# Performance work log

Hardware: AMD Instinct MI355X
Metric: run time of the kernel (lower is better)

The kernel has to match this reference:

```python
import jax, jax.numpy as jnp
import numpy as np

# dims: B batch, L residues, CS=c_s, N_EXP mHC streams, H heads, CH c_hidden,
# PQK/PV qk/v points, CZ=c_p pair channels, RANK z-factor rank, CZQ=CZ//4
B, L, CS, N_EXP, H, CH, PQK, PV, CZ, RANK = 4, 1024, 384, 4, 8, 64, 4, 8, 128, 2
CZQ = CZ // 4
SINKHORN_ITERS = 20


def quat_to_rot(q):
    q = q / jnp.sqrt((q * q).sum(-1, keepdims=True) + 1e-8)
    w, x, y, z = q[..., 0], q[..., 1], q[..., 2], q[..., 3]
    R = jnp.stack([
        1 - 2 * (y * y + z * z), 2 * (x * y - w * z), 2 * (x * z + w * y),
        2 * (x * y + w * z), 1 - 2 * (x * x + z * z), 2 * (y * z - w * x),
        2 * (x * z - w * y), 2 * (y * z + w * x), 1 - 2 * (x * x + y * y)], axis=-1)
    return R.reshape(q.shape[:-1] + (3, 3))


def layer_norm(x, g, b, eps=1e-5):
    mu = x.mean(-1, keepdims=True)
    var = ((x - mu) ** 2).mean(-1, keepdims=True)
    return (x - mu) * jax.lax.rsqrt(var + eps) * g + b


def sinkhorn(logits):
    # project onto doubly-stochastic matrices (Birkhoff polytope), fixed iters
    M = jnp.exp(logits - logits.max(axis=(-2, -1), keepdims=True))
    for _ in range(SINKHORN_ITERS):
        M = M / (M.sum(-1, keepdims=True) + 1e-8)
        M = M / (M.sum(-2, keepdims=True) + 1e-8)
    return M


def _forward(s, z_factor_1, z_factor_2, quat_t, trans, mask, b_pre, b_post, b_res,
             W_pre, W_post, W_res, alpha, Wq, Wk, Wv, Wq_pts, Wk_pts, Wv_pts,
             Wz_q, Wz_k, head_w, Wo, bo, ln1_g, ln1_b, Wt1, bt1, Wt2, bt2,
             Wt3, bt3, lnt_g, lnt_b, Wbb, bbb):
    # --- mHC: expand_input (first layer replicates stream) + dynamic mappings ---
    s_exp = jnp.broadcast_to(s[:, :, None, :], (B, L, N_EXP, CS))
    h = s_exp.reshape(B, L, N_EXP * CS)
    hn = h * jax.lax.rsqrt((h * h).mean(-1, keepdims=True) + 1e-6)
    H_pre = jax.nn.softmax(b_pre + alpha * (hn @ W_pre), -1)        # [B,L,n]
    H_post = 2.0 * jax.nn.sigmoid(b_post + alpha * (hn @ W_post))   # [B,L,n]
    H_res = sinkhorn(b_res + alpha * (hn @ W_res).reshape(B, L, N_EXP, N_EXP))
    s_c = jnp.einsum('bln,blnc->blc', H_pre, s_exp)                 # contraction

    rot = quat_to_rot(quat_t)                                       # [B,L,3,3]

    # --- Flash-IPA (dense math-equivalent reference) ---
    q = (s_c @ Wq).reshape(B, L, H, CH)
    k = (s_c @ Wk).reshape(B, L, H, CH)
    v = (s_c @ Wv).reshape(B, L, H, CH)
    qp = (s_c @ Wq_pts).reshape(B, L, H, PQK, 3)
    kp = (s_c @ Wk_pts).reshape(B, L, H, PQK, 3)
    vp = (s_c @ Wv_pts).reshape(B, L, H, PV, 3)

    def to_global(p):
        return jnp.einsum('blij,blhpj->blhpi', rot, p) + trans[:, :, None, None, :]

    qp_g, kp_g, vp_g = to_global(qp), to_global(kp), to_global(vp)

    # low-rank factorized pair bias (z = outer product of per-residue factors)
    zq = jnp.einsum('blrz,zh->blrh', z_factor_1, Wz_q)
    zk = jnp.einsum('blrz,zh->blrh', z_factor_1, Wz_k)
    bias = jnp.einsum('birh,bjrh->bhij', zq, zk)

    qk = jnp.einsum('bihc,bjhc->bhij', q, k) / np.sqrt(CH)
    qn = (qp_g ** 2).sum((-2, -1)).transpose(0, 2, 1)               # [B,H,L]
    kn = (kp_g ** 2).sum((-2, -1)).transpose(0, 2, 1)
    pdot = jnp.einsum('bihpd,bjhpd->bhij', qp_g, kp_g)
    d2 = qn[:, :, :, None] + kn[:, :, None, :] - 2.0 * pdot         # sum_p ||qp_i - kp_j||^2
    gamma = jax.nn.softplus(head_w)
    wC = np.sqrt(2.0 / (9.0 * PQK))
    wL = np.sqrt(1.0 / 3.0)
    logits = wL * (qk + bias) - (wL * wC * 0.5) * gamma[None, :, None, None] * d2
    logits = jnp.where(mask[:, None, None, :] > 0, logits, -1e9)
    a = jax.nn.softmax(logits, -1)

    o = jnp.einsum('bhij,bjhc->bihc', a, v).reshape(B, L, H * CH)
    opt_g = jnp.einsum('bhij,bjhpd->bihpd', a, vp_g)
    diff = opt_g - trans[:, :, None, None, :]
    opt_l = jnp.einsum('blij,blhpi->blhpj', rot, diff)              # R^T (x - t)
    opt_norm = jnp.sqrt((opt_l ** 2).sum(-1) + 1e-8)
    opair = jnp.einsum('bhij,bjhrc->bihrc', a, z_factor_2).reshape(B, L, H * RANK * CZQ)
    feat = jnp.concatenate([o, opt_l.reshape(B, L, H * PV * 3),
                            opt_norm.reshape(B, L, H * PV), opair], -1)
    ipa_out = feat @ Wo + bo

    # residual + (dropout=identity at eval) + LN + transition (residual MLP) + LN
    s1 = layer_norm(s_c + ipa_out, ln1_g, ln1_b)
    t1 = jax.nn.relu(s1 @ Wt1 + bt1)
    t2 = jax.nn.relu(t1 @ Wt2 + bt2)
    s_ipa = layer_norm(s1 + (t2 @ Wt3 + bt3), lnt_g, lnt_b)

    # backbone update: quaternion (1,b,c,d) + translation, composed with frame
    upd = s_ipa @ Wbb + bbb                                         # [B,L,6]
    quat_u = jnp.concatenate([jnp.ones((B, L, 1), upd.dtype), upd[..., :3]], -1)
    R_u = quat_to_rot(quat_u)
    rot_new = jnp.einsum('blij,bljk->blik', rot, R_u)
    trans_new = jnp.einsum('blij,blj->bli', rot, upd[..., 3:]) + trans

    # mHC combine: H_res @ s  +  H_post^T * s_ipa (broadcast over streams)
    s_out = jnp.einsum('blmn,blnc->blmc', H_res, s_exp) + H_post[..., None] * s_ipa[:, :, None, :]
    return s_out, rot_new, trans_new


def setup_inputs() -> dict:
    key = jax.random.key(0)
    ks = jax.random.split(key, 24)

    def nrm(k, shape, scale=1.0):
        return jax.random.normal(k, shape, jnp.float32) * scale

    FEAT = H * CH + H * PV * 4 + H * RANK * CZQ  # 512 + 256 + 512 = 1280
    return dict(
        s=nrm(ks[0], (B, L, CS)),
        z_factor_1=nrm(ks[1], (B, L, RANK, CZ)),
        z_factor_2=nrm(ks[2], (B, L, H, RANK, CZQ)),
        quat_t=nrm(ks[3], (B, L, 4)),
        trans=nrm(ks[4], (B, L, 3)),
        mask=jnp.ones((B, L), jnp.float32),
        b_pre=nrm(ks[5], (N_EXP,), 0.02),
        b_post=nrm(ks[6], (N_EXP,), 0.02),
        b_res=nrm(ks[7], (N_EXP, N_EXP), 0.02),
        W_pre=nrm(ks[8], (N_EXP * CS, N_EXP), 0.02),
        W_post=nrm(ks[9], (N_EXP * CS, N_EXP), 0.02),
        W_res=nrm(ks[10], (N_EXP * CS, N_EXP * N_EXP), 0.02),
        alpha=jnp.float32(0.01),
        Wq=nrm(ks[11], (CS, H * CH), 0.02),
        Wk=nrm(ks[12], (CS, H * CH), 0.02),
        Wv=nrm(ks[13], (CS, H * CH), 0.02),
        Wq_pts=nrm(ks[14], (CS, H * PQK * 3), 0.02),
        Wk_pts=nrm(ks[15], (CS, H * PQK * 3), 0.02),
        Wv_pts=nrm(ks[16], (CS, H * PV * 3), 0.02),
        Wz_q=nrm(ks[17], (CZ, H), 0.02),
        Wz_k=nrm(ks[18], (CZ, H), 0.02),
        head_w=jnp.zeros((H,), jnp.float32),
        Wo=nrm(ks[19], (FEAT, CS), 0.02),
        bo=jnp.zeros((CS,), jnp.float32),
        ln1_g=jnp.ones((CS,), jnp.float32),
        ln1_b=jnp.zeros((CS,), jnp.float32),
        Wt1=nrm(ks[20], (CS, CS), 0.02),
        bt1=jnp.zeros((CS,), jnp.float32),
        Wt2=nrm(ks[21], (CS, CS), 0.02),
        bt2=jnp.zeros((CS,), jnp.float32),
        Wt3=nrm(ks[22], (CS, CS), 0.02),
        bt3=jnp.zeros((CS,), jnp.float32),
        lnt_g=jnp.ones((CS,), jnp.float32),
        lnt_b=jnp.zeros((CS,), jnp.float32),
        Wbb=nrm(ks[23], (CS, 6), 0.02),
        bbb=jnp.zeros((6,), jnp.float32),
    )


def reference(s, z_factor_1, z_factor_2, quat_t, trans, mask, b_pre, b_post, b_res,
              W_pre, W_post, W_res, alpha, Wq, Wk, Wv, Wq_pts, Wk_pts, Wv_pts,
              Wz_q, Wz_k, head_w, Wo, bo, ln1_g, ln1_b, Wt1, bt1, Wt2, bt2,
              Wt3, bt3, lnt_g, lnt_b, Wbb, bbb):
    return _forward(s, z_factor_1, z_factor_2, quat_t, trans, mask, b_pre, b_post,
                    b_res, W_pre, W_post, W_res, alpha, Wq, Wk, Wv, Wq_pts, Wk_pts,
                    Wv_pts, Wz_q, Wz_k, head_w, Wo, bo, ln1_g, ln1_b, Wt1, bt1,
                    Wt2, bt2, Wt3, bt3, lnt_g, lnt_b, Wbb, bbb)
```

## Files before the change

### kernel.cpp

```cpp
#include <hip/hip_runtime.h>
#include <hip/hip_bf16.h>

typedef __hip_bfloat16 bf16;
typedef float f4v __attribute__((ext_vector_type(4)));
typedef short s8v __attribute__((ext_vector_type(8)));

#define CSD    384
#define LL     1024
#define NH     8
#define BL     4096
#define NPROJ  1920
#define QDP    96
#define VDP    160
#define FEATD  1280

#define OFF_S      0
#define OFF_QUAT   1572864
#define OFF_TRANS  1589248
#define OFF_MASK   1601536
#define OFF_BPOST  1605632
#define OFF_BRES   1605648
#define OFF_WPOST  1605664
#define OFF_WRES   1611808
#define OFF_ALPHA  1636384
#define OFF_WQ     1636400
#define OFF_WK     1833008
#define OFF_WV     2029616
#define OFF_WQP    2226224
#define OFF_WKP    2263088
#define OFF_WVP    2299952
#define OFF_WZQ    2373680
#define OFF_WZK    2374704
#define OFF_HEADW  2375728
#define OFF_WO     2375744
#define OFF_BO     2867264
#define OFF_LN1G   2867648
#define OFF_LN1B   2868032
#define OFF_WT1    2868416
#define OFF_BT1    3015872
#define OFF_WT2    3016256
#define OFF_BT2    3163712
#define OFF_WT3    3164096
#define OFF_BT3    3311552
#define OFF_LNTG   3311936
#define OFF_LNTB   3312320
#define OFF_WBB    3312704
#define OFF_BBB    3315008
#define IN_END     3315024

#define WS_FLAG    3315024
#define WS_WPOSTR  3315040
#define WS_WRESR   3316576
#define WS_HPOST   3322720
#define WS_ROWSUM  3339104
#define WS_ROTB    3355488
#define WS_WCATT   3392352
#define WS_WOT     3760992
#define WS_WT1T    4006752
#define WS_WT2T    4080480
#define WS_WT3T    4154208
#define WS_PROJ    4227936
#define WS_QB      12092256
#define WS_KB      13665120
#define WS_VT      15237984

#define OUT_ROT 6291456
#define OUT_TR  6328320

#define NSEG 32

struct P36 { const void* p[36]; };

__device__ __forceinline__ float b2f(bf16 x) { return __bfloat162float(x); }

__device__ __forceinline__ short f2bs(float x) {
  unsigned u = __float_as_uint(x);
  u += 0x7FFFu + ((u >> 16) & 1u);
  return (short)(u >> 16);
}

__device__ __forceinline__ int packbf(float lo, float hi) {
  return (int)(unsigned short)f2bs(lo) | ((int)f2bs(hi) << 16);
}

__device__ __forceinline__ float ldraw(const void* p, size_t i, int flag) {
  return flag ? b2f(((const bf16*)p)[i]) : ((const float*)p)[i];
}

__device__ __forceinline__ float wredf(float v) {
#pragma unroll
  for (int o = 1; o < 64; o <<= 1) v += __shfl_xor(v, o, 64);
  return v;
}

__global__ void detect_k(const unsigned int* __restrict__ mask_raw, int* __restrict__ flag) {
  if (threadIdx.x == 0 && blockIdx.x == 0) flag[0] = (mask_raw[0] == 0x3F803F80u) ? 1 : 0;
}

__global__ __launch_bounds__(256) void cvtall_k(P36 ptrs, float* __restrict__ dst, const int* __restrict__ flagp) {
  const int i = blockIdx.x * 256 + threadIdx.x;
  if (i >= IN_END) return;
  const int flag = flagp[0];
  const int seg_src_t[NSEG] = {0,3,4,5,7,8,10,11,12,13,14,15,16,17,18,19,20,21,22,23,24,25,26,27,28,29,30,31,32,33,34,35};
  const int seg_dst_t[NSEG] = {OFF_S,OFF_QUAT,OFF_TRANS,OFF_MASK,OFF_BPOST,OFF_BRES,OFF_WPOST,OFF_WRES,OFF_ALPHA,
                               OFF_WQ,OFF_WK,OFF_WV,OFF_WQP,OFF_WKP,OFF_WVP,OFF_WZQ,OFF_WZK,OFF_HEADW,
                               OFF_WO,OFF_BO,OFF_LN1G,OFF_LN1B,OFF_WT1,OFF_BT1,OFF_WT2,OFF_BT2,OFF_WT3,OFF_BT3,
                               OFF_LNTG,OFF_LNTB,OFF_WBB,OFF_BBB};
  const int seg_cnt_t[NSEG] = {1572864,16384,12288,4096,4,16,6144,24576,1,
                               196608,196608,196608,36864,36864,73728,1024,1024,8,
                               491520,384,384,384,147456,384,147456,384,147456,384,
                               384,384,2304,6};
  int off = i, cnt = seg_cnt_t[0];
  const void* sp = ptrs.p[0];
#pragma unroll
  for (int k = 1; k < NSEG; k++) {
    if (i >= seg_dst_t[k]) { off = i - seg_dst_t[k]; cnt = seg_cnt_t[k]; sp = ptrs.p[seg_src_t[k]]; }
  }
  float v = 0.f;
  if (off < cnt) v = flag ? b2f(((const bf16*)sp)[off]) : ((const float*)sp)[off];
  dst[i] = v;
}

__global__ __launch_bounds__(256) void wprep_k(const float* __restrict__ ws, short* __restrict__ wsS) {
  const int jobs_src[10] = {OFF_WQ, OFF_WK, OFF_WV, OFF_WQP, OFF_WKP, OFF_WVP, OFF_WO, OFF_WT1, OFF_WT2, OFF_WT3};
  const int jobs_dst[10] = {WS_WCATT*2, WS_WCATT*2 + 512*384, WS_WCATT*2 + 1024*384, WS_WCATT*2 + 1536*384,
                            WS_WCATT*2 + 1632*384, WS_WCATT*2 + 1728*384, WS_WOT*2, WS_WT1T*2, WS_WT2T*2, WS_WT3T*2};
  const int jobs_K[10] = {384,384,384,384,384,384,1280,384,384,384};
  const int jobs_N[10] = {512,512,512,96,96,192,384,384,384,384};
  const int jobs_t0[10] = {0,192,384,576,612,648,720,1200,1344,1488};
  const int t = blockIdx.x;
  int j = 0;
#pragma unroll
  for (int k = 1; k < 10; k++) if (t >= jobs_t0[k]) j = k;
  const int tl = t - jobs_t0[j];
  const int K = jobs_K[j], N = jobs_N[j];
  const int ntn = N >> 5;
  const int kt = tl / ntn, nt = tl - kt * ntn;
  const int k0 = kt * 32, n0 = nt * 32;
  const float* src = ws + jobs_src[j];
  short* dst = wsS + jobs_dst[j];
  __shared__ float T[32][36];
  {
    const int r = threadIdx.x >> 3, cq = (threadIdx.x & 7) * 4;
    const float4 a = *(const float4*)(src + (size_t)(k0 + r) * N + n0 + cq);
    T[r][cq] = a.x; T[r][cq + 1] = a.y; T[r][cq + 2] = a.z; T[r][cq + 3] = a.w;
  }
  __syncthreads();
  {
    const int n = threadIdx.x >> 3, kq = (threadIdx.x & 7) * 4;
    short pk4[4];
#pragma unroll
    for (int e = 0; e < 4; e++) pk4[e] = f2bs(T[kq + e][n]);
    *(int2*)(dst + (size_t)(n0 + n) * K + k0 + kq) = *(const int2*)pk4;
  }
}

__global__ __launch_bounds__(256) void wreduce_k(const float* __restrict__ Wpost, const float* __restrict__ Wres,
                                                 float* __restrict__ WpostR, float* __restrict__ WresR) {
  int i = blockIdx.x * 256 + threadIdx.x;
  if (i < CSD * 4) {
    int c = i >> 2, n = i & 3;
    float s = 0.f;
#pragma unroll
    for (int blk = 0; blk < 4; blk++) s += Wpost[(blk * CSD + c) * 4 + n];
    WpostR[i] = s;
  }
  if (i < CSD * 16) {
    int c = i >> 4, n = i & 15;
    float s = 0.f;
#pragma unroll
    for (int blk = 0; blk < 4; blk++) s += Wres[(blk * CSD + c) * 16 + n];
    WresR[i] = s;
  }
}

__global__ __launch_bounds__(64) void mhc_k(const float* __restrict__ sF, const float* __restrict__ quat,
                                            const float* __restrict__ bpost, const float* __restrict__ bres,
                                            const float* __restrict__ alpha_p, const float* __restrict__ WpostR,
                                            const float* __restrict__ WresR, float* __restrict__ hpost,
                                            float* __restrict__ rowsum, float* __restrict__ rotb) {
  const int bl = blockIdx.x, t = threadIdx.x;
  const float* sr = sF + (size_t)bl * CSD;
  float ssq = 0.f, dp[4] = {0.f, 0.f, 0.f, 0.f}, dr[16];
#pragma unroll
  for (int n = 0; n < 16; n++) dr[n] = 0.f;
#pragma unroll
  for (int e = 0; e < 6; e++) {
    const int c = t + e * 64;
    const float sv = sr[c];
    ssq = fmaf(sv, sv, ssq);
#pragma unroll
    for (int n = 0; n < 4; n++) dp[n] = fmaf(sv, WpostR[c * 4 + n], dp[n]);
#pragma unroll
    for (int n = 0; n < 16; n++) dr[n] = fmaf(sv, WresR[c * 16 + n], dr[n]);
  }
  ssq = wredf(ssq);
#pragma unroll
  for (int n = 0; n < 4; n++) dp[n] = wredf(dp[n]);
#pragma unroll
  for (int n = 0; n < 16; n++) dr[n] = wredf(dr[n]);
  const float alpha = alpha_p[0];
  const float invn = rsqrtf(ssq * (1.f / 384.f) + 1e-6f);
  if (t == 0) {
#pragma unroll
    for (int n = 0; n < 4; n++) {
      const float x = bpost[n] + alpha * invn * dp[n];
      hpost[bl * 4 + n] = 2.f / (1.f + __expf(-x));
    }
    float M[16];
    float mx = -1e30f;
#pragma unroll
    for (int k = 0; k < 16; k++) { M[k] = bres[k] + alpha * invn * dr[k]; mx = fmaxf(mx, M[k]); }
#pragma unroll
    for (int k = 0; k < 16; k++) M[k] = __expf(M[k] - mx);
    for (int it = 0; it < 20; it++) {
#pragma unroll
      for (int r = 0; r < 4; r++) {
        const float s4 = M[r * 4] + M[r * 4 + 1] + M[r * 4 + 2] + M[r * 4 + 3];
        const float iv = 1.f / (s4 + 1e-8f);
        M[r * 4] *= iv; M[r * 4 + 1] *= iv; M[r * 4 + 2] *= iv; M[r * 4 + 3] *= iv;
      }
#pragma unroll
      for (int c2 = 0; c2 < 4; c2++) {
        const float s4 = M[c2] + M[4 + c2] + M[8 + c2] + M[12 + c2];
        const float iv = 1.f / (s4 + 1e-8f);
        M[c2] *= iv; M[4 + c2] *= iv; M[8 + c2] *= iv; M[12 + c2] *= iv;
      }
    }
#pragma unroll
    for (int r = 0; r < 4; r++)
      rowsum[bl * 4 + r] = M[r * 4] + M[r * 4 + 1] + M[r * 4 + 2] + M[r * 4 + 3];
  }
  if (t == 1) {
    float w = quat[bl * 4 + 0], x = quat[bl * 4 + 1];
    float y = quat[bl * 4 + 2], z = quat[bl * 4 + 3];
    const float iq = rsqrtf(w * w + x * x + y * y + z * z + 1e-8f);
    w *= iq; x *= iq; y *= iq; z *= iq;
    float* R = rotb + (size_t)bl * 9;
    R[0] = 1.f - 2.f * (y * y + z * z); R[1] = 2.f * (x * y - w * z); R[2] = 2.f * (x * z + w * y);
    R[3] = 2.f * (x * y + w * z); R[4] = 1.f - 2.f * (x * x + z * z); R[5] = 2.f * (y * z - w * x);
    R[6] = 2.f * (x * z - w * y); R[7] = 2.f * (y * z + w * x); R[8] = 1.f - 2.f * (x * x + y * y);
  }
}

__global__ __launch_bounds__(256) void gemm_mfma_k(const float* __restrict__ A, const short* __restrict__ Bt,
                                                   const float* __restrict__ bias, float* __restrict__ C,
                                                   int M, int N, int K, int relu) {
  __shared__ __align__(16) short As[128 * 40];
  __shared__ __align__(16) short Bs[128 * 40];
  const int tid = threadIdx.x;
  const int wid = tid >> 6, lane = tid & 63;
  const int c15 = lane & 15, q = lane >> 4;
  const int bm = blockIdx.y, bn = blockIdx.x;
  const int m_wave = (wid & 1) * 64, n_wave = (wid >> 1) * 64;
  const float* Ab = A + (size_t)(bm * 128) * K;
  const short* Bb = Bt + (size_t)(bn * 128) * K;

  f4v acc[4][4];
#pragma unroll
  for (int mi = 0; mi < 4; mi++)
#pragma unroll
    for (int ni = 0; ni < 4; ni++) acc[mi][ni] = (f4v){0.f, 0.f, 0.f, 0.f};

  for (int k0 = 0; k0 < K; k0 += 32) {
    __syncthreads();
#pragma unroll
    for (int e = 0; e < 4; e++) {
      const int slot = tid + e * 256;
      const int m = slot >> 3, k4 = (slot & 7) * 4;
      const float4 a = *(const float4*)(Ab + (size_t)m * K + k0 + k4);
      short pk[4] = {f2bs(a.x), f2bs(a.y), f2bs(a.z), f2bs(a.w)};
      *(int2*)&As[m * 40 + k4] = *(const int2*)pk;
    }
#pragma unroll
    for (int e = 0; e < 2; e++) {
      const int slot = tid + e * 256;
      const int n = slot >> 2, k8 = (slot & 3) * 8;
      *(int4*)&Bs[n * 40 + k8] = *(const int4*)(Bb + (size_t)n * K + k0 + k8);
    }
    __syncthreads();
    s8v Af[4], Bf[4];
#pragma unroll
    for (int mi = 0; mi < 4; mi++) Af[mi] = *(const s8v*)&As[(m_wave + mi * 16 + c15) * 40 + q * 8];
#pragma unroll
    for (int ni = 0; ni < 4; ni++) Bf[ni] = *(const s8v*)&Bs[(n_wave + ni * 16 + c15) * 40 + q * 8];
#pragma unroll
    for (int mi = 0; mi < 4; mi++)
#pragma unroll
      for (int ni = 0; ni < 4; ni++)
        acc[mi][ni] = __builtin_amdgcn_mfma_f32_16x16x32_bf16(Af[mi], Bf[ni], acc[mi][ni], 0, 0, 0);
  }
#pragma unroll
  for (int mi = 0; mi < 4; mi++) {
#pragma unroll
    for (int r = 0; r < 4; r++) {
      const int row = bm * 128 + m_wave + mi * 16 + q * 4 + r;
      float* Cr = C + (size_t)row * N + bn * 128 + n_wave;
#pragma unroll
      for (int ni = 0; ni < 4; ni++) {
        const int col = bn * 128 + n_wave + ni * 16 + c15;
        float v = acc[mi][ni][r];
        if (bias != nullptr) v += bias[col];
        if (relu) v = fmaxf(v, 0.f);
        Cr[ni * 16 + c15] = v;
      }
    }
  }
}

__global__ __launch_bounds__(64) void assemble_k(const float* __restrict__ proj, const float* __restrict__ rotb,
                                                 const float* __restrict__ trans, const void* __restrict__ z1raw,
                                                 const void* __restrict__ z2raw, const float* __restrict__ Wzq,
                                                 const float* __restrict__ Wzk, const float* __restrict__ headw,
                                                 const int* __restrict__ flagp, short* __restrict__ Qb,
                                                 short* __restrict__ Kb, short* __restrict__ Vtb) {
  __shared__ float qt[8][16], kt[8][16];
  const int bl = blockIdx.x, lane = threadIdx.x;
  const int h = lane >> 3, sub = lane & 7;
  const int flag = flagp[0];
  const float* pr = proj + (size_t)bl * NPROJ;
  const float* R = rotb + (size_t)bl * 9;
  const float txx = trans[bl * 3 + 0], tyy = trans[bl * 3 + 1], tzz = trans[bl * 3 + 2];
  float gamma;
  { const float w = headw[h]; gamma = (w > 20.f) ? w : log1pf(__expf(w)); }
  const float wL = 0.57735026918962576f;
  const float wC = 0.23570226039551584f;
  const float ch = wL * wC * 0.5f * gamma;
  const float qscale = wL * 0.125f;

  float zq0 = 0.f, zq1 = 0.f, zk0 = 0.f, zk1 = 0.f;
  const size_t zbase = (size_t)bl * 256;
  for (int zz = sub; zz < 128; zz += 8) {
    const float a0 = ldraw(z1raw, zbase + zz, flag);
    const float a1 = ldraw(z1raw, zbase + 128 + zz, flag);
    const float wq = Wzq[zz * 8 + h], wk = Wzk[zz * 8 + h];
    zq0 = fmaf(a0, wq, zq0); zq1 = fmaf(a1, wq, zq1);
    zk0 = fmaf(a0, wk, zk0); zk1 = fmaf(a1, wk, zk1);
  }
#pragma unroll
  for (int o = 1; o < 8; o <<= 1) {
    zq0 += __shfl_xor(zq0, o, 64); zq1 += __shfl_xor(zq1, o, 64);
    zk0 += __shfl_xor(zk0, o, 64); zk1 += __shfl_xor(zk1, o, 64);
  }

  const int b = bl >> 10, l = bl & 1023;
  const int bh = b * NH + h;
  const size_t row = (size_t)bh * LL + l;
  short* Q = Qb + row * QDP;
  short* Kx = Kb + row * QDP;

  {
    const float* ps = pr + h * 64 + sub * 8;
    const float4 a0 = ((const float4*)ps)[0], a1 = ((const float4*)ps)[1];
    int4 qi;
    qi.x = packbf(a0.x * qscale, a0.y * qscale); qi.y = packbf(a0.z * qscale, a0.w * qscale);
    qi.z = packbf(a1.x * qscale, a1.y * qscale); qi.w = packbf(a1.z * qscale, a1.w * qscale);
    ((int4*)Q)[sub] = qi;
    const float* pk = pr + 512 + h * 64 + sub * 8;
    const float4 b0 = ((const float4*)pk)[0], b1 = ((const float4*)pk)[1];
    int4 ki;
    ki.x = packbf(b0.x, b0.y); ki.y = packbf(b0.z, b0.w);
    ki.z = packbf(b1.x, b1.y); ki.w = packbf(b1.z, b1.w);
    ((int4*)Kx)[sub] = ki;
    const float* pv = pr + 1024 + h * 64 + sub * 8;
#pragma unroll
    for (int e = 0; e < 8; e++)
      Vtb[((size_t)bh * VDP + sub * 8 + e) * LL + l] = f2bs(pv[e]);
  }

  {
    const float* pp = pr + ((sub < 4) ? 1536 : 1632) + h * 12 + (sub & 3) * 3;
    const float gx = R[0] * pp[0] + R[1] * pp[1] + R[2] * pp[2] + txx;
    const float gy = R[3] * pp[0] + R[4] * pp[1] + R[5] * pp[2] + tyy;
    const float gz = R[6] * pp[0] + R[7] * pp[1] + R[8] * pp[2] + tzz;
    float nrm = gx * gx + gy * gy + gz * gz;
    nrm += __shfl_xor(nrm, 1, 64);
    nrm += __shfl_xor(nrm, 2, 64);
    const float other = __shfl_xor(nrm, 4, 64);
    const float qn = (sub < 4) ? nrm : other;
    const float kn = (sub < 4) ? other : nrm;
    if (sub < 4) {
      qt[h][2 + sub * 3 + 0] = 2.f * ch * gx;
      qt[h][2 + sub * 3 + 1] = 2.f * ch * gy;
      qt[h][2 + sub * 3 + 2] = 2.f * ch * gz;
    } else {
      kt[h][2 + (sub - 4) * 3 + 0] = gx;
      kt[h][2 + (sub - 4) * 3 + 1] = gy;
      kt[h][2 + (sub - 4) * 3 + 2] = gz;
    }
    if (sub == 0) {
      qt[h][0] = wL * zq0; qt[h][1] = wL * zq1; qt[h][14] = -ch * qn; qt[h][15] = 1.f;
      kt[h][0] = zk0;      kt[h][1] = zk1;      kt[h][14] = 1.f;      kt[h][15] = -ch * kn;
    }
  }
  {
    int4 z4; z4.x = 0; z4.y = 0; z4.z = 0; z4.w = 0;
    if (sub < 2) {
      const float* s4 = &qt[h][sub * 8];
      int4 qi;
      qi.x = packbf(s4[0], s4[1]); qi.y = packbf(s4[2], s4[3]);
      qi.z = packbf(s4[4], s4[5]); qi.w = packbf(s4[6], s4[7]);
      ((int4*)Q)[8 + sub] = qi;
    } else if (sub < 4) {
      const float* s4 = &kt[h][(sub - 2) * 8];
      int4 ki;
      ki.x = packbf(s4[0], s4[1]); ki.y = packbf(s4[2], s4[3]);
      ki.z = packbf(s4[4], s4[5]); ki.w = packbf(s4[6], s4[7]);
      ((int4*)Kx)[8 + sub - 2] = ki;
    } else if (sub == 4) ((int4*)Q)[10] = z4;
    else if (sub == 5) ((int4*)Q)[11] = z4;
    else if (sub == 6) ((int4*)Kx)[10] = z4;
    else ((int4*)Kx)[11] = z4;
  }
  {
    const float* pv3 = pr + 1728 + h * 24 + sub * 3;
    const float gx = R[0] * pv3[0] + R[1] * pv3[1] + R[2] * pv3[2] + txx;
    const float gy = R[3] * pv3[0] + R[4] * pv3[1] + R[5] * pv3[2] + tyy;
    const float gz = R[6] * pv3[0] + R[7] * pv3[1] + R[8] * pv3[2] + tzz;
    const int c = 64 + sub * 3;
    Vtb[((size_t)bh * VDP + c + 0) * LL + l] = f2bs(gx);
    Vtb[((size_t)bh * VDP + c + 1) * LL + l] = f2bs(gy);
    Vtb[((size_t)bh * VDP + c + 2) * LL + l] = f2bs(gz);
  }
  {
    const size_t z2base = ((size_t)bl * NH + h) * 64 + sub * 8;
#pragma unroll
    for (int e = 0; e < 8; e++)
      Vtb[((size_t)bh * VDP + 88 + sub * 8 + e) * LL + l] = f2bs(ldraw(z2raw, z2base + e, flag));
    Vtb[((size_t)bh * VDP + 152 + sub) * LL + l] = 0;
  }
}

__global__ __launch_bounds__(512, 2) void attn_k(const short* __restrict__ Qb, const short* __restrict__ Kb,
                                                 const short* __restrict__ Vtb, const float* __restrict__ maskF,
                                                 float* __restrict__ Oext) {
  __shared__ __align__(16) short smem[26624];
  short* Ks = smem;
  short* Vs = smem + 6656;
  short* Ps = smem + 19456;
  float* Msl = (float*)(smem + 24576);
  const int tid = threadIdx.x;
  const int wid = tid >> 6, lane = tid & 63;
  const int c15 = lane & 15, q = lane >> 4;
  const int blk = blockIdx.x;
  const int bh = blk & 31, qt2 = blk >> 5;
  const int b = bh >> 3, h = bh & 7;
  const int half = wid >> 2, mw = wid & 3;
  const int i0 = qt2 * 64 + mw * 16;

  const short* Kbase = Kb + (size_t)bh * LL * QDP;
  const short* Vbase = Vtb + (size_t)bh * VDP * LL;

  s8v Qa[3];
  const short* Qrow = Qb + ((size_t)bh * LL + i0 + c15) * QDP;
#pragma unroll
  for (int kc = 0; kc < 3; kc++) Qa[kc] = *(const s8v*)(Qrow + kc * 32 + q * 8);

  f4v Of[10];
#pragma unroll
  for (int vt = 0; vt < 10; vt++) Of[vt] = (f4v){0.f, 0.f, 0.f, 0.f};
  float mold[4] = {-1e30f, -1e30f, -1e30f, -1e30f};
  float lsum[4] = {0.f, 0.f, 0.f, 0.f};

  Msl[tid] = maskF[b * LL + tid];
  Msl[tid + 512] = maskF[b * LL + tid + 512];

  const int khs0 = tid / 384;
  const int kv0 = tid - khs0 * 384;
  const int krr0 = kv0 / 12, kcc0 = kv0 - krr0 * 12;
  int khs1 = 0, krr1 = 0, kcc1 = 0;
  if (tid < 256) { const int u = tid + 512; khs1 = u / 384; const int v2 = u - khs1 * 384; krr1 = v2 / 12; kcc1 = v2 - krr1 * 12; }
  const int vhs0 = tid / 640; const int vv0 = tid - vhs0 * 640; const int vcc0 = vv0 >> 2, vp0 = vv0 & 3;
  const int vhs1 = (tid + 512) / 640; const int vv1 = (tid + 512) - vhs1 * 640; const int vcc1 = vv1 >> 2, vp1 = vv1 & 3;
  int vhs2 = 0, vcc2 = 0, vp2 = 0;
  if (tid < 256) { const int u = tid + 1024; vhs2 = u / 640; const int v2 = u - vhs2 * 640; vcc2 = v2 >> 2; vp2 = v2 & 3; }

  int4 kr0, kr1, vr0, vr1, vr2;
  kr0 = *(const int4*)(Kbase + (size_t)(khs0 * 512 + krr0) * QDP + kcc0 * 8);
  if (tid < 256) kr1 = *(const int4*)(Kbase + (size_t)(khs1 * 512 + krr1) * QDP + kcc1 * 8);
  vr0 = *(const int4*)(Vbase + (size_t)vcc0 * LL + vhs0 * 512 + vp0 * 8);
  vr1 = *(const int4*)(Vbase + (size_t)vcc1 * LL + vhs1 * 512 + vp1 * 8);
  if (tid < 256) vr2 = *(const int4*)(Vbase + (size_t)vcc2 * LL + vhs2 * 512 + vp2 * 8);

  short* Ksl = Ks + half * 3328;
  short* Vsl = Vs + half * 6400;
  short* Pl = Ps + wid * 640;

  for (int jt = 0; jt < 16; jt++) {
    const int j0 = jt * 32;
    __syncthreads();
    *(int4*)&Ks[khs0 * 3328 + krr0 * 104 + kcc0 * 8] = kr0;
    if (tid < 256) *(int4*)&Ks[khs1 * 3328 + krr1 * 104 + kcc1 * 8] = kr1;
    *(int4*)&Vs[vhs0 * 6400 + vcc0 * 40 + vp0 * 8] = vr0;
    *(int4*)&Vs[vhs1 * 6400 + vcc1 * 40 + vp1 * 8] = vr1;
    if (tid < 256) *(int4*)&Vs[vhs2 * 6400 + vcc2 * 40 + vp2 * 8] = vr2;
    __syncthreads();
    if (jt < 15) {
      const int j0n = j0 + 32;
      kr0 = *(const int4*)(Kbase + (size_t)(khs0 * 512 + j0n + krr0) * QDP + kcc0 * 8);
      if (tid < 256) kr1 = *(const int4*)(Kbase + (size_t)(khs1 * 512 + j0n + krr1) * QDP + kcc1 * 8);
      vr0 = *(const int4*)(Vbase + (size_t)vcc0 * LL + vhs0 * 512 + j0n + vp0 * 8);
      vr1 = *(const int4*)(Vbase + (size_t)vcc1 * LL + vhs1 * 512 + j0n + vp1 * 8);
      if (tid < 256) vr2 = *(const int4*)(Vbase + (size_t)vcc2 * LL + vhs2 * 512 + j0n + vp2 * 8);
    }

    f4v Sf0 = (f4v){0.f, 0.f, 0.f, 0.f}, Sf1 = (f4v){0.f, 0.f, 0.f, 0.f};
#pragma unroll
    for (int kc = 0; kc < 3; kc++) {
      const s8v K0 = *(const s8v*)&Ksl[c15 * 104 + kc * 32 + q * 8];
      const s8v K1 = *(const s8v*)&Ksl[(16 + c15) * 104 + kc * 32 + q * 8];
      Sf0 = __builtin_amdgcn_mfma_f32_16x16x32_bf16(Qa[kc], K0, Sf0, 0, 0, 0);
      Sf1 = __builtin_amdgcn_mfma_f32_16x16x32_bf16(Qa[kc], K1, Sf1, 0, 0, 0);
    }
    const float mv0 = Msl[half * 512 + j0 + c15];
    const float mv1 = Msl[half * 512 + j0 + 16 + c15];
    float lg0[4], lg1[4], tm[4], p0[4], p1[4];
#pragma unroll
    for (int r = 0; r < 4; r++) {
      lg0[r] = (mv0 > 0.f) ? Sf0[r] : -1e9f;
      lg1[r] = (mv1 > 0.f) ? Sf1[r] : -1e9f;
      tm[r] = fmaxf(lg0[r], lg1[r]);
    }
#pragma unroll
    for (int r = 0; r < 4; r++) {
      tm[r] = fmaxf(tm[r], __shfl_xor(tm[r], 1, 64));
      tm[r] = fmaxf(tm[r], __shfl_xor(tm[r], 2, 64));
      tm[r] = fmaxf(tm[r], __shfl_xor(tm[r], 4, 64));
      tm[r] = fmaxf(tm[r], __shfl_xor(tm[r], 8, 64));
    }
    const bool need = (tm[0] > mold[0]) | (tm[1] > mold[1]) | (tm[2] > mold[2]) | (tm[3] > mold[3]);
    if (__any(need)) {
      float al[4];
#pragma unroll
      for (int r = 0; r < 4; r++) {
        const float mn = fmaxf(mold[r], tm[r]);
        al[r] = __expf(mold[r] - mn);
        mold[r] = mn;
        p0[r] = __expf(lg0[r] - mn);
        p1[r] = __expf(lg1[r] - mn);
        lsum[r] = lsum[r] * al[r] + p0[r] + p1[r];
      }
#pragma unroll
      for (int vt = 0; vt < 10; vt++) {
#pragma unroll
        for (int r = 0; r < 4; r++) Of[vt][r] *= al[r];
      }
    } else {
#pragma unroll
      for (int r = 0; r < 4; r++) {
        p0[r] = __expf(lg0[r] - mold[r]);
        p1[r] = __expf(lg1[r] - mold[r]);
        lsum[r] += p0[r] + p1[r];
      }
    }
#pragma unroll
    for (int r = 0; r < 4; r++) {
      Pl[(q * 4 + r) * 40 + c15] = f2bs(p0[r]);
      Pl[(q * 4 + r) * 40 + 16 + c15] = f2bs(p1[r]);
    }
    const s8v Pa = *(const s8v*)&Pl[c15 * 40 + q * 8];
#pragma unroll
    for (int vt = 0; vt < 10; vt++) {
      const s8v Vf = *(const s8v*)&Vsl[(vt * 16 + c15) * 40 + q * 8];
      Of[vt] = __builtin_amdgcn_mfma_f32_16x16x32_bf16(Pa, Vf, Of[vt], 0, 0, 0);
    }
  }
#pragma unroll
  for (int r = 0; r < 4; r++) {
    lsum[r] += __shfl_xor(lsum[r], 1, 64);
    lsum[r] += __shfl_xor(lsum[r], 2, 64);
    lsum[r] += __shfl_xor(lsum[r], 4, 64);
    lsum[r] += __shfl_xor(lsum[r], 8, 64);
  }
  float* Obuf = (float*)smem;
  float* Mbuf = (float*)(smem + 20480);
  float* Lbuf = Mbuf + 64;
  __syncthreads();
  if (half == 1) {
#pragma unroll
    for (int r = 0; r < 4; r++) {
      const int rowi = mw * 16 + q * 4 + r;
#pragma unroll
      for (int vt = 0; vt < 10; vt++) Obuf[rowi * 160 + vt * 16 + c15] = Of[vt][r];
      if (c15 == 0) { Mbuf[rowi] = mold[r]; Lbuf[rowi] = lsum[r]; }
    }
  }
  __syncthreads();
  if (half == 0) {
#pragma unroll
    for (int r = 0; r < 4; r++) {
      const int rowi = mw * 16 + q * 4 + r;
      const float m2 = Mbuf[rowi], l2 = Lbuf[rowi];
      const float mx = fmaxf(mold[r], m2);
      const float a1 = __expf(mold[r] - mx), a2 = __expf(m2 - mx);
      const float inv = 1.f / (lsum[r] * a1 + l2 * a2);
      const int i = i0 + q * 4 + r;
      float* Or = Oext + ((size_t)(b * LL + i) * NH + h) * VDP;
#pragma unroll
      for (int vt = 0; vt < 10; vt++)
        Or[vt * 16 + c15] = (Of[vt][r] * a1 + Obuf[rowi * 160 + vt * 16 + c15] * a2) * inv;
    }
  }
}

__global__ __launch_bounds__(64) void feat_k(const float* __restrict__ Oext, const float* __restrict__ rotb,
                                             const float* __restrict__ trans, float* __restrict__ feat) {
  const int bl = blockIdx.x, lane = threadIdx.x;
  const int h = lane >> 3, sub = lane & 7;
  const float* O = Oext + ((size_t)bl * 8 + h) * VDP;
  float* f = feat + (size_t)bl * FEATD;
  {
    const float4 a0 = ((const float4*)(O + sub * 8))[0], a1 = ((const float4*)(O + sub * 8))[1];
    ((float4*)(f + h * 64 + sub * 8))[0] = a0;
    ((float4*)(f + h * 64 + sub * 8))[1] = a1;
    const float4 z0 = ((const float4*)(O + 88 + sub * 8))[0], z1 = ((const float4*)(O + 88 + sub * 8))[1];
    ((float4*)(f + 768 + h * 64 + sub * 8))[0] = z0;
    ((float4*)(f + 768 + h * 64 + sub * 8))[1] = z1;
  }
  const float* R = rotb + (size_t)bl * 9;
  const float txx = trans[bl * 3 + 0], tyy = trans[bl * 3 + 1], tzz = trans[bl * 3 + 2];
  {
    const float dx = O[64 + sub * 3 + 0] - txx;
    const float dy = O[64 + sub * 3 + 1] - tyy;
    const float dz = O[64 + sub * 3 + 2] - tzz;
    const float lx = R[0] * dx + R[3] * dy + R[6] * dz;
    const float ly = R[1] * dx + R[4] * dy + R[7] * dz;
    const float lz = R[2] * dx + R[5] * dy + R[8] * dz;
    f[512 + h * 24 + sub * 3 + 0] = lx;
    f[512 + h * 24 + sub * 3 + 1] = ly;
    f[512 + h * 24 + sub * 3 + 2] = lz;
    f[704 + h * 8 + sub] = sqrtf(lx * lx + ly * ly + lz * lz + 1e-8f);
  }
}

__global__ __launch_bounds__(64) void ln_k(const float* __restrict__ x, const float* __restrict__ resid,
                                           const float* __restrict__ g, const float* __restrict__ bta,
                                           float* __restrict__ out) {
  const int row = blockIdx.x, t = threadIdx.x;
  const float* xr = x + (size_t)row * CSD;
  const float* rr = resid + (size_t)row * CSD;
  float v[6];
  float s = 0.f;
#pragma unroll
  for (int e = 0; e < 6; e++) {
    const int c = t + e * 64;
    v[e] = xr[c] + rr[c];
    s += v[e];
  }
  s = wredf(s);
  const float mu = s * (1.f / 384.f);
  float var = 0.f;
#pragma unroll
  for (int e = 0; e < 6; e++) { const float d = v[e] - mu; var = fmaf(d, d, var); }
  var = wredf(var) * (1.f / 384.f);
  const float inv = rsqrtf(var + 1e-5f);
#pragma unroll
  for (int e = 0; e < 6; e++) {
    const int c = t + e * 64;
    out[(size_t)row * CSD + c] = (v[e] - mu) * inv * g[c] + bta[c];
  }
}

__global__ __launch_bounds__(64) void lnfinal_k(const float* __restrict__ x , const float* __restrict__ resid ,
                                                const float* __restrict__ g, const float* __restrict__ bta,
                                                const float* __restrict__ sF, const float* __restrict__ rotb,
                                                const float* __restrict__ trans, const float* __restrict__ hpost,
                                                const float* __restrict__ rowsum, const float* __restrict__ Wbb,
                                                const float* __restrict__ bbb, const int* __restrict__ flagp,
                                                void* __restrict__ outv) {
  const int bl = blockIdx.x, t = threadIdx.x;
  const int flag = flagp[0];
  bf16* outb = (bf16*)outv;
  float* outf = (float*)outv;
  const float* xr = x + (size_t)bl * CSD;
  const float* rr = resid + (size_t)bl * CSD;
  float v[6];
  float s = 0.f;
#pragma unroll
  for (int e = 0; e < 6; e++) {
    const int c = t + e * 64;
    v[e] = xr[c] + rr[c];
    s += v[e];
  }
  s = wredf(s);
  const float mu = s * (1.f / 384.f);
  float var = 0.f;
#pragma unroll
  for (int e = 0; e < 6; e++) { const float d = v[e] - mu; var = fmaf(d, d, var); }
  var = wredf(var) * (1.f / 384.f);
  const float inv = rsqrtf(var + 1e-5f);
  float si6[6];
#pragma unroll
  for (int e = 0; e < 6; e++) {
    const int c = t + e * 64;
    si6[e] = (v[e] - mu) * inv * g[c] + bta[c];
  }
  float d6[6] = {0.f, 0.f, 0.f, 0.f, 0.f, 0.f};
#pragma unroll
  for (int e = 0; e < 6; e++) {
    const int c = t + e * 64;
#pragma unroll
    for (int u = 0; u < 6; u++) d6[u] = fmaf(si6[e], Wbb[c * 6 + u], d6[u]);
  }
#pragma unroll
  for (int u = 0; u < 6; u++) d6[u] = wredf(d6[u]);
  float upd[6];
#pragma unroll
  for (int u = 0; u < 6; u++) upd[u] = d6[u] + bbb[u];
  const float* R = rotb + (size_t)bl * 9;
  if (t == 0) {
    float w = 1.f, x2 = upd[0], y = upd[1], z = upd[2];
    const float iq = rsqrtf(w * w + x2 * x2 + y * y + z * z + 1e-8f);
    w *= iq; x2 *= iq; y *= iq; z *= iq;
    const float Ru[9] = {1.f - 2.f * (y * y + z * z), 2.f * (x2 * y - w * z), 2.f * (x2 * z + w * y),
                         2.f * (x2 * y + w * z), 1.f - 2.f * (x2 * x2 + z * z), 2.f * (y * z - w * x2),
                         2.f * (x2 * z - w * y), 2.f * (y * z + w * x2), 1.f - 2.f * (x2 * x2 + y * y)};
#pragma unroll
    for (int i = 0; i < 3; i++)
#pragma unroll
      for (int j = 0; j < 3; j++) {
        const float rv = R[i * 3 + 0] * Ru[0 + j] + R[i * 3 + 1] * Ru[3 + j] + R[i * 3 + 2] * Ru[6 + j];
        const size_t o = OUT_ROT + (size_t)bl * 9 + i * 3 + j;
        if (flag) outb[o] = __float2bfloat16(rv); else outf[o] = rv;
      }
#pragma unroll
    for (int i = 0; i < 3; i++) {
      const float tv = R[i * 3 + 0] * upd[3] + R[i * 3 + 1] * upd[4] + R[i * 3 + 2] * upd[5] + trans[bl * 3 + i];
      const size_t o = OUT_TR + (size_t)bl * 3 + i;
      if (flag) outb[o] = __float2bfloat16(tv); else outf[o] = tv;
    }
  }
  const float hp0 = hpost[bl * 4 + 0], hp1 = hpost[bl * 4 + 1], hp2 = hpost[bl * 4 + 2], hp3 = hpost[bl * 4 + 3];
  const float rs0 = rowsum[bl * 4 + 0], rs1 = rowsum[bl * 4 + 1], rs2 = rowsum[bl * 4 + 2], rs3 = rowsum[bl * 4 + 3];
  const float* sr = sF + (size_t)bl * CSD;
#pragma unroll
  for (int e = 0; e < 6; e++) {
    const int c = t + e * 64;
    const float sv = sr[c], sp = si6[e];
    const size_t base = (size_t)bl * 4 * CSD + c;
    const float o0 = rs0 * sv + hp0 * sp;
    const float o1 = rs1 * sv + hp1 * sp;
    const float o2 = rs2 * sv + hp2 * sp;
    const float o3 = rs3 * sv + hp3 * sp;
    if (flag) {
      outb[base + 0 * CSD] = __float2bfloat16(o0);
      outb[base + 1 * CSD] = __float2bfloat16(o1);
      outb[base + 2 * CSD] = __float2bfloat16(o2);
      outb[base + 3 * CSD] = __float2bfloat16(o3);
    } else {
      outf[base + 0 * CSD] = o0;
      outf[base + 1 * CSD] = o1;
      outf[base + 2 * CSD] = o2;
      outf[base + 3 * CSD] = o3;
    }
  }
}

extern "C" void kernel_launch(void* const* d_in, const int* in_sizes, int n_in,
                              void* d_out, int out_size, void* d_ws, size_t ws_size,
                              hipStream_t stream) {
  float* ws = (float*)d_ws;
  int* flag = (int*)(ws + WS_FLAG);

  P36 ptrs;
  for (int i = 0; i < 36; i++) ptrs.p[i] = d_in[i];

  float* sF     = ws + OFF_S;
  float* WpostR = ws + WS_WPOSTR;
  float* WresR  = ws + WS_WRESR;
  float* hpost  = ws + WS_HPOST;
  float* rowsum = ws + WS_ROWSUM;
  float* rotb   = ws + WS_ROTB;
  short* WcatT  = (short*)(ws + WS_WCATT);
  short* WoT    = (short*)(ws + WS_WOT);
  short* Wt1T   = (short*)(ws + WS_WT1T);
  short* Wt2T   = (short*)(ws + WS_WT2T);
  short* Wt3T   = (short*)(ws + WS_WT3T);
  float* proj   = ws + WS_PROJ;
  short* Qb     = (short*)(ws + WS_QB);
  short* Kb     = (short*)(ws + WS_KB);
  short* Vtb    = (short*)(ws + WS_VT);
  float* Oext   = ws + WS_PROJ;
  float* featb  = ws + WS_QB;
  float* x1s1   = ws + WS_PROJ;
  float* t1b    = ws + WS_PROJ + 1572864;
  float* t2b    = ws + WS_PROJ + 3145728;
  float* x3     = ws + WS_PROJ + 4718592;

  detect_k<<<1, 64, 0, stream>>>((const unsigned int*)d_in[5], flag);
  cvtall_k<<<(IN_END + 255) / 256, 256, 0, stream>>>(ptrs, ws, flag);
  wprep_k<<<1632, 256, 0, stream>>>(ws, (short*)ws);
  wreduce_k<<<24, 256, 0, stream>>>(ws + OFF_WPOST, ws + OFF_WRES, WpostR, WresR);
  mhc_k<<<BL, 64, 0, stream>>>(sF, ws + OFF_QUAT, ws + OFF_BPOST, ws + OFF_BRES, ws + OFF_ALPHA,
                               WpostR, WresR, hpost, rowsum, rotb);
  gemm_mfma_k<<<dim3(15, 32), 256, 0, stream>>>(sF, WcatT, nullptr, proj, BL, NPROJ, CSD, 0);
  assemble_k<<<BL, 64, 0, stream>>>(proj, rotb, ws + OFF_TRANS, d_in[1], d_in[2],
                                    ws + OFF_WZQ, ws + OFF_WZK, ws + OFF_HEADW, flag, Qb, Kb, Vtb);
  attn_k<<<512, 512, 0, stream>>>(Qb, Kb, Vtb, ws + OFF_MASK, Oext);
  feat_k<<<BL, 64, 0, stream>>>(Oext, rotb, ws + OFF_TRANS, featb);
  gemm_mfma_k<<<dim3(3, 32), 256, 0, stream>>>(featb, WoT, ws + OFF_BO, x1s1, BL, CSD, FEATD, 0);
  ln_k<<<BL, 64, 0, stream>>>(x1s1, sF, ws + OFF_LN1G, ws + OFF_LN1B, x1s1);
  gemm_mfma_k<<<dim3(3, 32), 256, 0, stream>>>(x1s1, Wt1T, ws + OFF_BT1, t1b, BL, CSD, CSD, 1);
  gemm_mfma_k<<<dim3(3, 32), 256, 0, stream>>>(t1b, Wt2T, ws + OFF_BT2, t2b, BL, CSD, CSD, 1);
  gemm_mfma_k<<<dim3(3, 32), 256, 0, stream>>>(t2b, Wt3T, ws + OFF_BT3, x3, BL, CSD, CSD, 0);
  lnfinal_k<<<BL, 64, 0, stream>>>(x3, x1s1, ws + OFF_LNTG, ws + OFF_LNTB, sF, rotb,
                                   ws + OFF_TRANS, hpost, rowsum, ws + OFF_WBB, ws + OFF_BBB,
                                   flag, d_out);
}
```

Baseline: 482.3 us.

## Write V row-major in assemble_k and transpose via LDS in new kernel

assemble_k used to write V directly in transposed layout with scattered 2-byte stores at stride LL. It now packs V rows into 16-byte vector stores in a row-major staging buffer. A new vtrans_k kernel then transposes each 64-row tile through shared memory into the layout attn_k expects. This trades uncoalesced scattered stores for one extra kernel launch and an extra read and write of V.

```diff
diff --git a/kernel.cpp b/kernel.cpp
--- a/kernel.cpp
+++ b/kernel.cpp
@@ -63,6 +63,7 @@
 #define WS_QB      12092256
 #define WS_KB      13665120
 #define WS_VT      15237984
+#define WS_VROW    17859424
 
 #define OUT_ROT 6291456
 #define OUT_TR  6328320
@@ -313,8 +314,8 @@
                                                  const void* __restrict__ z2raw, const float* __restrict__ Wzq,
                                                  const float* __restrict__ Wzk, const float* __restrict__ headw,
                                                  const int* __restrict__ flagp, short* __restrict__ Qb,
-                                                 short* __restrict__ Kb, short* __restrict__ Vtb) {
-  __shared__ float qt[8][16], kt[8][16];
+                                                 short* __restrict__ Kb, short* __restrict__ Vrow) {
+  __shared__ float qt[8][16], kt[8][16], vt[8][24];
   const int bl = blockIdx.x, lane = threadIdx.x;
   const int h = lane >> 3, sub = lane & 7;
   const int flag = flagp[0];
@@ -348,6 +349,7 @@
   const size_t row = (size_t)bh * LL + l;
   short* Q = Qb + row * QDP;
   short* Kx = Kb + row * QDP;
+  short* Vo = Vrow + row * VDP;
 
   {
     const float* ps = pr + h * 64 + sub * 8;
@@ -363,9 +365,11 @@
     ki.z = packbf(b1.x, b1.y); ki.w = packbf(b1.z, b1.w);
     ((int4*)Kx)[sub] = ki;
     const float* pv = pr + 1024 + h * 64 + sub * 8;
-#pragma unroll
-    for (int e = 0; e < 8; e++)
-      Vtb[((size_t)bh * VDP + sub * 8 + e) * LL + l] = f2bs(pv[e]);
+    const float4 v0 = ((const float4*)pv)[0], v1 = ((const float4*)pv)[1];
+    int4 vi;
+    vi.x = packbf(v0.x, v0.y); vi.y = packbf(v0.z, v0.w);
+    vi.z = packbf(v1.x, v1.y); vi.w = packbf(v1.z, v1.w);
+    ((int4*)Vo)[sub] = vi;
   }
 
   {
@@ -394,6 +398,13 @@
     }
   }
   {
+    const float* pv3 = pr + 1728 + h * 24 + sub * 3;
+    const float gx = R[0] * pv3[0] + R[1] * pv3[1] + R[2] * pv3[2] + txx;
+    const float gy = R[3] * pv3[0] + R[4] * pv3[1] + R[5] * pv3[2] + tyy;
+    const float gz = R[6] * pv3[0] + R[7] * pv3[1] + R[8] * pv3[2] + tzz;
+    vt[h][sub * 3 + 0] = gx; vt[h][sub * 3 + 1] = gy; vt[h][sub * 3 + 2] = gz;
+  }
+  {
     int4 z4; z4.x = 0; z4.y = 0; z4.z = 0; z4.w = 0;
     if (sub < 2) {
       const float* s4 = &qt[h][sub * 8];
@@ -411,23 +422,46 @@
     else if (sub == 5) ((int4*)Q)[11] = z4;
     else if (sub == 6) ((int4*)Kx)[10] = z4;
     else ((int4*)Kx)[11] = z4;
-  }
-  {
-    const float* pv3 = pr + 1728 + h * 24 + sub * 3;
-    const float gx = R[0] * pv3[0] + R[1] * pv3[1] + R[2] * pv3[2] + txx;
-    const float gy = R[3] * pv3[0] + R[4] * pv3[1] + R[5] * pv3[2] + tyy;
-    const float gz = R[6] * pv3[0] + R[7] * pv3[1] + R[8] * pv3[2] + tzz;
-    const int c = 64 + sub * 3;
-    Vtb[((size_t)bh * VDP + c + 0) * LL + l] = f2bs(gx);
-    Vtb[((size_t)bh * VDP + c + 1) * LL + l] = f2bs(gy);
-    Vtb[((size_t)bh * VDP + c + 2) * LL + l] = f2bs(gz);
+    if (sub < 3) {
+      const float* s4 = &vt[h][sub * 8];
+      int4 vi;
+      vi.x = packbf(s4[0], s4[1]); vi.y = packbf(s4[2], s4[3]);
+      vi.z = packbf(s4[4], s4[5]); vi.w = packbf(s4[6], s4[7]);
+      ((int4*)Vo)[8 + sub] = vi;
+    } else if (sub == 3) {
+      ((int4*)Vo)[19] = z4;
+    }
   }
   {
     const size_t z2base = ((size_t)bl * NH + h) * 64 + sub * 8;
-#pragma unroll
-    for (int e = 0; e < 8; e++)
-      Vtb[((size_t)bh * VDP + 88 + sub * 8 + e) * LL + l] = f2bs(ldraw(z2raw, z2base + e, flag));
-    Vtb[((size_t)bh * VDP + 152 + sub) * LL + l] = 0;
+    float z[8];
+#pragma unroll
+    for (int e = 0; e < 8; e++) z[e] = ldraw(z2raw, z2base + e, flag);
+    int4 vi;
+    vi.x = packbf(z[0], z[1]); vi.y = packbf(z[2], z[3]);
+    vi.z = packbf(z[4], z[5]); vi.w = packbf(z[6], z[7]);
+    ((int4*)Vo)[11 + sub] = vi;
+  }
+}
+
+__global__ __launch_bounds__(256) void vtrans_k(const short* __restrict__ Vrow, short* __restrict__ Vtb) {
+  __shared__ __align__(16) short T[64 * 168];
+  const int tid = threadIdx.x;
+  const int bh = blockIdx.y;
+  const int l0 = blockIdx.x * 64;
+  const short* src = Vrow + (size_t)bh * LL * VDP + (size_t)l0 * VDP;
+  for (int u = tid; u < 1280; u += 256) {
+    const int ll = u / 20, j = u % 20;
+    *(int4*)&T[ll * 168 + j * 8] = *(const int4*)(src + (size_t)ll * VDP + j * 8);
+  }
+  __syncthreads();
+  short* dst = Vtb + (size_t)bh * VDP * LL + l0;
+  for (int u = tid; u < 1280; u += 256) {
+    const int c = u >> 3, seg = u & 7;
+    short tmp[8];
+#pragma unroll
+    for (int e = 0; e < 8; e++) tmp[e] = T[(seg * 8 + e) * 168 + c];
+    *(int4*)(dst + (size_t)c * LL + seg * 8) = *(const int4*)tmp;
   }
 }
 
@@ -780,6 +814,7 @@
   short* Qb     = (short*)(ws + WS_QB);
   short* Kb     = (short*)(ws + WS_KB);
   short* Vtb    = (short*)(ws + WS_VT);
+  short* Vrow   = (short*)(ws + WS_VROW);
   float* Oext   = ws + WS_PROJ;
   float* featb  = ws + WS_QB;
   float* x1s1   = ws + WS_PROJ;
@@ -795,7 +830,8 @@
                                WpostR, WresR, hpost, rowsum, rotb);
   gemm_mfma_k<<<dim3(15, 32), 256, 0, stream>>>(sF, WcatT, nullptr, proj, BL, NPROJ, CSD, 0);
   assemble_k<<<BL, 64, 0, stream>>>(proj, rotb, ws + OFF_TRANS, d_in[1], d_in[2],
-                                    ws + OFF_WZQ, ws + OFF_WZK, ws + OFF_HEADW, flag, Qb, Kb, Vtb);
+                                    ws + OFF_WZQ, ws + OFF_WZK, ws + OFF_HEADW, flag, Qb, Kb, Vrow);
+  vtrans_k<<<dim3(16, 32), 256, 0, stream>>>(Vrow, Vtb);
   attn_k<<<512, 512, 0, stream>>>(Qb, Kb, Vtb, ws + OFF_MASK, Oext);
   feat_k<<<BL, 64, 0, stream>>>(Oext, rotb, ws + OFF_TRANS, featb);
   gemm_mfma_k<<<dim3(3, 32), 256, 0, stream>>>(featb, WoT, ws + OFF_BO, x1s1, BL, CSD, FEATD, 0);
```

After: 459.5 us. 1.05x faster.
